# Performance work log

Hardware: AMD Instinct MI355X
Metric: run time of the kernel (lower is better)

## Reference

```python
import jax, jax.numpy as jnp
import numpy as np

WIDTH = 1024
NH = 16
HD = 64
MBS = 16
B = 4
L = 2048
BASE_LR = 1.0
EPS = 1e-6


def gelu_tanh(x):
    return jax.nn.gelu(x, approximate=True)


def gelu_bwd(x):
    t = jnp.tanh(0.79788456 * x * (1 + 0.044715 * x * x))
    return 0.5 * x * ((1 - t * t) * (0.79788456 + 0.1070322243 * x * x)) + 0.5 * (1 + t)


def ln_fwd(x, g, b):
    mu = x.mean(-1, keepdims=True)
    var = ((x - mu) ** 2).mean(-1, keepdims=True)
    return g * ((x - mu) * jax.lax.rsqrt(var + EPS)) + b


def ln_l2_bwd(x, tgt, g, b):
    # grad of 0.5*||LN(x)-tgt||^2 wrt x
    mu = x.mean(-1, keepdims=True)
    var = ((x - mu) ** 2).mean(-1, keepdims=True)
    std = jnp.sqrt(var + EPS)
    xh = (x - mu) / std
    gx = (g * xh + b - tgt) * g
    return (gx - gx.mean(-1, keepdims=True) - xh * (gx * xh).mean(-1, keepdims=True)) / std


def adapter_forward(hidden_states, Wq, Wk, Wv, Wo, Wg, lr_w, lr_b,
                    learnable_token_idx, norm_w, norm_b, W1, b1, W2, b2,
                    post_w, post_b):
    Bb, Ll, width = hidden_states.shape
    nh, hd = norm_w.shape
    mbs = learnable_token_idx.shape[0]
    nc = Ll // mbs  # L chosen divisible by mini_batch_size

    def split_heads(x):  # [B,L,width] -> [B,nh,nc,mbs,hd]
        return x.reshape(Bb, Ll, nh, hd).transpose(0, 2, 1, 3).reshape(Bb, nh, nc, mbs, hd)

    XQ = split_heads(hidden_states @ Wq.T)
    XK = split_heads(hidden_states @ Wk.T)
    XV = split_heads(hidden_states @ Wv.T)

    # eta: learnable per-token lr gate (get_eta)
    X = hidden_states.reshape(Bb, nc, mbs, width)
    lr = jnp.einsum('bnkc,hdc->bhnkd', X, lr_w) + lr_b.reshape(1, nh, 1, 1, 1)
    lr = jax.nn.sigmoid(lr).transpose(0, 1, 2, 4, 3)  # [B,nh,nc,1,mbs]
    lr_eta = BASE_LR * lr / hd
    token_idx = jnp.clip(1.0 / jnp.arange(1, mbs + 1, dtype=hidden_states.dtype)
                         + learnable_token_idx, 0.0, None)
    token_eta = token_idx.reshape(1, 1, 1, mbs, 1)
    eta = token_eta * lr_eta  # [B,nh,nc,mbs,mbs]

    tril = jnp.tril(jnp.ones((mbs, mbs), dtype=hidden_states.dtype))
    lnw = norm_w.reshape(nh, 1, hd)
    lnb = norm_b.reshape(nh, 1, hd)

    def step(carry, xs):
        W1s, b1s, W2s, b2s = carry  # [B,nh,hd,4hd], [B,nh,1,4hd], [B,nh,4hd,hd], [B,nh,1,hd]
        XQm, XKm, XVm, etam = xs    # [B,nh,mbs,hd] x3, [B,nh,mbs,mbs]
        X1 = XKm
        Z1 = X1 @ W1s + b1s
        X2 = gelu_tanh(Z1)
        Z2 = X2 @ W2s + b2s
        gZ2 = ln_l2_bwd(Z2, XVm - XKm, lnw, lnb)
        gZ1 = (gZ2 @ jnp.swapaxes(W2s, -1, -2)) * gelu_bwd(Z1)
        eta_tril = etam * tril
        Attn1 = tril * (XQm @ jnp.swapaxes(X1, -1, -2))
        b1_bar = b1s - eta_tril @ gZ1
        Z1_bar = XQm @ W1s - (etam * Attn1) @ gZ1 + b1_bar
        X2_bar = gelu_tanh(Z1_bar)
        Attn2 = tril * (X2_bar @ jnp.swapaxes(X2, -1, -2))
        b2_bar = b2s - eta_tril @ gZ2
        Z2_bar = X2_bar @ W2s - (etam * Attn2) @ gZ2 + b2_bar
        last = etam[:, :, -1, :, None]  # [B,nh,mbs,1]
        W1n = W1s - jnp.swapaxes(last * X1, -1, -2) @ gZ1
        b1n = b1s - (last * gZ1).sum(-2, keepdims=True)
        W2n = W2s - jnp.swapaxes(last * X2, -1, -2) @ gZ2
        b2n = b2s - (last * gZ2).sum(-2, keepdims=True)
        XQW = XQm + ln_fwd(Z2_bar, lnw, lnb)
        return (W1n, b1n, W2n, b2n), XQW

    carry0 = (jnp.broadcast_to(W1, (Bb,) + W1.shape),
              jnp.broadcast_to(b1, (Bb,) + b1.shape),
              jnp.broadcast_to(W2, (Bb,) + W2.shape),
              jnp.broadcast_to(b2, (Bb,) + b2.shape))
    xs = tuple(jnp.moveaxis(t, 2, 0) for t in (XQ, XK, XV, eta))
    _, XQW = jax.lax.scan(step, carry0, xs)  # [nc,B,nh,mbs,hd]
    out = XQW.transpose(1, 0, 3, 2, 4).reshape(Bb, Ll, width)

    # post_norm (LayerNorm eps=1e-6)
    out = ln_fwd(out, post_w, post_b)
    # gate
    out = gelu_tanh(hidden_states @ Wg.T) * out
    # o_proj
    return out @ Wo.T


def setup_inputs():
    key = jax.random.key(0)
    ks = jax.random.split(key, 10)
    n = lambda k, s: jax.random.normal(k, s, dtype=jnp.float32) * 0.02
    return {
        'hidden_states': jax.random.normal(ks[0], (B, L, WIDTH), dtype=jnp.float32),
        'Wq': n(ks[1], (WIDTH, WIDTH)),
        'Wk': n(ks[2], (WIDTH, WIDTH)),
        'Wv': n(ks[3], (WIDTH, WIDTH)),
        'Wo': n(ks[4], (WIDTH, WIDTH)),
        'Wg': n(ks[5], (WIDTH, WIDTH)),
        'lr_w': n(ks[6], (NH, 1, WIDTH)),
        'lr_b': jnp.zeros((NH, 1), jnp.float32),
        'learnable_token_idx': jnp.zeros((MBS,), jnp.float32),
        'norm_w': jnp.ones((NH, HD), jnp.float32),
        'norm_b': jnp.zeros((NH, HD), jnp.float32),
        'W1': n(ks[7], (NH, HD, 4 * HD)),
        'b1': jnp.zeros((NH, 1, 4 * HD), jnp.float32),
        'W2': n(ks[8], (NH, 4 * HD, HD)),
        'b2': jnp.zeros((NH, 1, HD), jnp.float32),
        'post_w': jnp.ones((WIDTH,), jnp.float32),
        'post_b': jnp.zeros((WIDTH,), jnp.float32),
    }


def reference(hidden_states, Wq, Wk, Wv, Wo, Wg, lr_w, lr_b, learnable_token_idx,
              norm_w, norm_b, W1, b1, W2, b2, post_w, post_b):
    return adapter_forward(hidden_states, Wq, Wk, Wv, Wo, Wg, lr_w, lr_b,
                           learnable_token_idx, norm_w, norm_b, W1, b1, W2, b2,
                           post_w, post_b)
```

## Files before the change

kernel.cpp:

```cpp
#include <hip/hip_runtime.h>

#define WIDTH 1024
#define MBSZ 16
#define LLL 2048
#define NCHUNK 128

typedef __attribute__((ext_vector_type(4))) float f32x4;
typedef __attribute__((ext_vector_type(2))) float f32x2;
typedef __attribute__((ext_vector_type(8))) short short8;
typedef __attribute__((ext_vector_type(4))) short short4v;
typedef __attribute__((ext_vector_type(2))) unsigned u32x2;
typedef __attribute__((ext_vector_type(4))) unsigned u32x4;

#define MFMA16(a, b, c) __builtin_amdgcn_mfma_f32_16x16x32_bf16((a), (b), (c), 0, 0, 0)

__device__ __forceinline__ short f2bf(float f) {
  unsigned u = __float_as_uint(f);
  u = (u + 0x7FFFu + ((u >> 16) & 1u)) >> 16;
  return (short)u;
}
__device__ __forceinline__ float bf2f(short s) {
  return __uint_as_float(((unsigned)(unsigned short)s) << 16);
}
__device__ __forceinline__ unsigned cvt_pk(float lo, float hi) {
  unsigned r;
  asm("v_cvt_pk_bf16_f32 %0, %1, %2" : "=v"(r) : "v"(lo), "v"(hi));
  return r;
}
__device__ __forceinline__ float fast_e2u(float x) {
  return __builtin_amdgcn_exp2f(x * (2.30220776f + 0.10294322f * x * x));
}
__device__ __forceinline__ float gelu_f(float x) {
  float e = fast_e2u(x);
  return x * (1.0f - __builtin_amdgcn_rcpf(e + 1.0f));
}
__device__ __forceinline__ float gelu_bwd_f(float x) {
  float e = fast_e2u(x);
  float r = __builtin_amdgcn_rcpf(e + 1.0f);
  return 2.0f * x * r * (1.0f - r) * (0.79788456f + 0.1070322243f * x * x) + (1.0f - r);
}
__device__ __forceinline__ int w2row(int d) { return d * 264 + (d >> 3) * 24; }

template <int OUTBF>
__device__ __forceinline__ void gemm_64x128(const short* __restrict__ A,
                                            const short* __restrict__ W,
                                            float* __restrict__ C,
                                            short* __restrict__ Cb,
                                            int m0, int n0,
                                            short* sA, short* sB, int t2) {
  const int wv = t2 >> 6, ln = t2 & 63;
  const int fr = ln & 15, kh = (ln >> 4) * 8;
  const int arow = t2 >> 2, aseg = (t2 & 3) * 8;
  f32x4 acc[8];
#pragma unroll
  for (int s = 0; s < 8; ++s) acc[s] = (f32x4){0.f, 0.f, 0.f, 0.f};
  const short* ga = A + (long)(m0 + arow) * 1024 + aseg;
  const short* gw0 = W + (long)(n0 + arow) * 1024 + aseg;
  const short* gw1 = W + (long)(n0 + 64 + arow) * 1024 + aseg;
  for (int k0 = 0; k0 < 1024; k0 += 32) {
    const short8 a8 = *(const short8*)(ga + k0);
    const short8 w80 = *(const short8*)(gw0 + k0);
    const short8 w81 = *(const short8*)(gw1 + k0);
    *(short8*)&sA[arow * 40 + aseg] = a8;
    *(short8*)&sB[arow * 40 + aseg] = w80;
    *(short8*)&sB[(arow + 64) * 40 + aseg] = w81;
    __syncthreads();
    const short8 af = *(const short8*)&sA[(wv * 16 + fr) * 40 + kh];
#pragma unroll
    for (int s = 0; s < 8; ++s) {
      const short8 bf8 = *(const short8*)&sB[(s * 16 + fr) * 40 + kh];
      acc[s] = MFMA16(af, bf8, acc[s]);
    }
    __syncthreads();
  }
  const int orow = m0 + wv * 16 + (ln >> 4) * 4;
#pragma unroll
  for (int s = 0; s < 8; ++s)
#pragma unroll
    for (int q = 0; q < 4; ++q) {
      const long off = (long)(orow + q) * 1024 + n0 + s * 16 + fr;
      if (OUTBF) Cb[off] = f2bf(acc[s][q]);
      else C[off] = acc[s][q];
    }
}

__global__ __launch_bounds__(256) void cvt_kernel(const float* __restrict__ hs,
                                                  const float* __restrict__ Wq,
                                                  const float* __restrict__ Wk,
                                                  const float* __restrict__ Wv,
                                                  const float* __restrict__ Wg,
                                                  const float* __restrict__ Wo,
                                                  short* __restrict__ dst) {
  const long idx = ((long)blockIdx.x * 256 + threadIdx.x) * 8;
  if (idx >= 13631488L) return;
  const float* src;
  long off;
  if (idx < 8388608L)       { src = hs; off = idx; }
  else if (idx < 9437184L)  { src = Wq; off = idx - 8388608L; }
  else if (idx < 10485760L) { src = Wk; off = idx - 9437184L; }
  else if (idx < 11534336L) { src = Wv; off = idx - 10485760L; }
  else if (idx < 12582912L) { src = Wg; off = idx - 11534336L; }
  else                      { src = Wo; off = idx - 12582912L; }
  const f32x4 a = *(const f32x4*)(src + off);
  const f32x4 b = *(const f32x4*)(src + off + 4);
  u32x4 o;
  o[0] = cvt_pk(a[0], a[1]); o[1] = cvt_pk(a[2], a[3]);
  o[2] = cvt_pk(b[0], b[1]); o[3] = cvt_pk(b[2], b[3]);
  *(u32x4*)(dst + idx) = o;
}

__global__ __launch_bounds__(256) void gemm_final(const short* __restrict__ A,
                                                  const short* __restrict__ W,
                                                  float* __restrict__ C) {
  __shared__ __align__(16) short sA[2560];
  __shared__ __align__(16) short sB[5120];
  gemm_64x128<0>(A, W, C, nullptr, blockIdx.x * 64, blockIdx.y * 128, sA, sB, threadIdx.x);
}

__global__ __launch_bounds__(256) void qkv_lr_kernel(const short* __restrict__ hsb,
                                                     const short* __restrict__ Wqb,
                                                     const short* __restrict__ Wkb,
                                                     const short* __restrict__ Wvb,
                                                     float* __restrict__ Qb,
                                                     float* __restrict__ Kb,
                                                     float* __restrict__ Vb,
                                                     const float* __restrict__ hs,
                                                     const float* __restrict__ lrw,
                                                     const float* __restrict__ lrb,
                                                     float* __restrict__ LRb) {
  __shared__ __align__(16) short sA[2560];
  __shared__ __align__(16) short sB[5120];
  __shared__ __align__(16) float row[1024];
  const int tid = threadIdx.x;
  const int idx = blockIdx.x;
  if (idx < 3072) {
    const int which = idx >> 10, t = idx & 1023;
    const short* W = (which == 0) ? Wqb : (which == 1) ? Wkb : Wvb;
    float* C = (which == 0) ? Qb : (which == 1) ? Kb : Vb;
    gemm_64x128<0>(hsb, W, C, nullptr, (t & 127) * 64, (t >> 7) * 128, sA, sB, tid);
  } else {
    const int t = idx - 3072;
    *(f32x4*)&row[tid * 4] = *(const f32x4*)&hs[(long)t * 1024 + tid * 4];
    __syncthreads();
    const int hh = tid >> 4, j = tid & 15;
    const float* wrow = lrw + hh * 1024;
    float s = 0.f;
#pragma unroll 4
    for (int m = 0; m < 16; ++m) {
      const int c = j * 4 + m * 64;
      f32x4 x = *(const f32x4*)&row[c];
      f32x4 w = *(const f32x4*)&wrow[c];
      s += x[0] * w[0] + x[1] * w[1] + x[2] * w[2] + x[3] * w[3];
    }
#pragma unroll
    for (int o = 8; o; o >>= 1) s += __shfl_xor(s, o, 16);
    if (j == 0) {
      const float v = s + lrb[hh];
      const float sg = 1.f / (1.f + expf(-v));
      const int b = t >> 11, tr = t & 2047;
      LRb[((b << 4) + hh) * 2048 + tr] = sg * (1.f / 64.f);
    }
  }
}

__global__ __launch_bounds__(512, 2) void scan_gate_kernel(
    float* __restrict__ Qb, const float* __restrict__ Kb, const float* __restrict__ Vb,
    const float* __restrict__ LRb, const float* __restrict__ lti,
    const float* __restrict__ nw, const float* __restrict__ nb,
    const float* __restrict__ W1in, const float* __restrict__ b1in,
    const float* __restrict__ W2in, const float* __restrict__ b2in,
    const short* __restrict__ hsA, const short* __restrict__ Wgb,
    short* __restrict__ Gout) {
  __shared__ __align__(16) short sW1b[256 * 72];
  __shared__ __align__(16) short sW2dp[64 * 264 + 192];
  __shared__ __align__(16) short la1T[64 * 24];
  __shared__ __align__(16) short la2T[256 * 24];
  __shared__ __align__(16) short sX1b[16 * 72];
  __shared__ __align__(16) short sXQb[16 * 72];
  __shared__ __align__(16) float sXQf[16 * 68];
  __shared__ __align__(16) float sTg[16 * 72];
  __shared__ __align__(16) short sX2b[16 * 264];
  __shared__ __align__(16) short sXbb[16 * 264];
  __shared__ __align__(16) short sG1c[256 * 24];
  __shared__ __align__(16) short sG2b[16 * 72];
  __shared__ __align__(16) short sG2c[64 * 24];
  __shared__ __align__(16) float sZ2p0[16 * 68];
  __shared__ __align__(16) float sZ2p1[16 * 68];
  __shared__ __align__(16) float sZ2f[16 * 68];
  __shared__ __align__(16) short sC1b[16 * 24];
  __shared__ __align__(16) short sC2b[16 * 24];
  __shared__ __align__(16) float sB1[256];
  __shared__ __align__(16) float sB2[64];
  __shared__ float sLr[16];
  __shared__ float sTok[16];
  __shared__ __align__(16) float sLnw[64];
  __shared__ __align__(16) float sLnb[64];

  const int tid = threadIdx.x;

  if (blockIdx.x >= 64) {
    const int hh = tid >> 8, t2 = tid & 255;
    const int tile = (blockIdx.x - 64) * 2 + hh;
    short* sAh = sW1b + hh * 7680;
    short* sBh = sAh + 2560;
    gemm_64x128<1>(hsA, Wgb, nullptr, Gout, (tile & 127) * 64, (tile >> 7) * 128, sAh, sBh, t2);
    return;
  }

  const int bh = blockIdx.x, b = bh >> 4, h = bh & 15;
  const int w = tid >> 6, ln = tid & 63;
  const int fr = ln & 15, half = ln >> 4, hk = half * 8;
  const int nt0 = 2 * w;

  float w1m[8][4], w2m[8][4];
#pragma unroll
  for (int r = 0; r < 8; ++r) {
    const int T = w * 8 + r, dt = T >> 4, pt = T & 15;
#pragma unroll
    for (int qq = 0; qq < 4; ++qq) {
      w1m[r][qq] = W1in[h * 16384 + (dt * 16 + half * 4 + qq) * 256 + pt * 16 + fr];
      w2m[r][qq] = W2in[h * 16384 + (pt * 16 + half * 4 + qq) * 64 + dt * 16 + fr];
    }
  }
  for (int e = tid; e < 16384; e += 512) {
    {
      const int d = e >> 8, p = e & 255;
      sW1b[p * 72 + d] = f2bf(W1in[h * 16384 + e]);
    }
    {
      const int p = e >> 6, d = e & 63;
      sW2dp[w2row(d) + (p ^ (((d >> 3) & 3) << 3))] = f2bf(W2in[h * 16384 + e]);
    }
  }
  if (tid < 256) sB1[tid] = b1in[h * 256 + tid];
  if (tid < 64) { sB2[tid] = b2in[h * 64 + tid]; sLnw[tid] = nw[h * 64 + tid]; sLnb[tid] = nb[h * 64 + tid]; }
  if (tid < 16) sTok[tid] = fmaxf(1.0f / (float)(tid + 1) + lti[tid], 0.0f);

  const f32x4 zf4 = (f32x4){0.f, 0.f, 0.f, 0.f};
  short8 zs8;
#pragma unroll
  for (int j = 0; j < 8; ++j) zs8[j] = 0;

  const int pf_i = tid >> 5;
  const int pf_d = (tid & 31) * 2;
  f32x2 pk, pq, pv;
  float plr = 0.f;
  {
    const long a0 = ((long)(b * LLL + pf_i)) * WIDTH + h * 64 + pf_d;
    pk = *(const f32x2*)&Kb[a0];
    pq = *(const f32x2*)&Qb[a0];
    pv = *(const f32x2*)&Vb[a0];
    if (tid < 16) plr = LRb[(long)bh * 2048 + tid];
  }

  for (int n = 0; n < NCHUNK; ++n) {
    const long gbase = ((long)(b * LLL + n * MBSZ)) * WIDTH + h * 64;

    {
      *(unsigned*)&sX1b[pf_i * 72 + pf_d] = cvt_pk(pk[0], pk[1]);
      *(unsigned*)&sXQb[pf_i * 72 + pf_d] = cvt_pk(pq[0], pq[1]);
      sXQf[pf_i * 68 + pf_d] = pq[0];
      sXQf[pf_i * 68 + pf_d + 1] = pq[1];
      sTg[pf_i * 72 + pf_d] = pv[0] - pk[0];
      sTg[pf_i * 72 + pf_d + 1] = pv[1] - pk[1];
      if (tid < 16) sLr[tid] = plr;
    }
    __syncthreads();

    short8 aX1[2], aXQ[2];
    aX1[0] = *(const short8*)&sX1b[fr * 72 + hk];
    aX1[1] = *(const short8*)&sX1b[fr * 72 + 32 + hk];
    aXQ[0] = *(const short8*)&sXQb[fr * 72 + hk];
    aXQ[1] = *(const short8*)&sXQb[fr * 72 + 32 + hk];
    f32x4 z1[2], q1[2];
    float b1p[2];
#pragma unroll
    for (int t = 0; t < 2; ++t) {
      const int p = (nt0 + t) * 16 + fr;
      z1[t] = zf4; q1[t] = zf4;
#pragma unroll
      for (int ks = 0; ks < 2; ++ks) {
        short8 bw = *(const short8*)&sW1b[p * 72 + ks * 32 + hk];
        z1[t] = MFMA16(aX1[ks], bw, z1[t]);
        q1[t] = MFMA16(aXQ[ks], bw, q1[t]);
      }
      b1p[t] = sB1[p];
#pragma unroll
      for (int qq = 0; qq < 4; ++qq) {
        z1[t][qq] += b1p[t];
        sX2b[(half * 4 + qq) * 264 + p] = f2bf(gelu_f(z1[t][qq]));
      }
    }
    {
      const float tok15 = sTok[15];
      const int d = tid >> 3, j0 = (tid & 7) * 2;
      const float v0 = bf2f(sX1b[j0 * 72 + d]) * (tok15 * sLr[j0]);
      const float v1 = bf2f(sX1b[(j0 + 1) * 72 + d]) * (tok15 * sLr[j0 + 1]);
      *(unsigned*)&la1T[d * 24 + j0] = cvt_pk(v0, v1);
    }
    if (w == 0) {
      f32x4 c = MFMA16(aXQ[0], aX1[0], zf4);
      c = MFMA16(aXQ[1], aX1[1], c);
#pragma unroll
      for (int qq = 0; qq < 4; ++qq) {
        const int i = half * 4 + qq, j = fr;
        sC1b[i * 24 + j] = f2bf((i >= j) ? sTok[i] * sLr[j] * (c[qq] + 1.0f) : 0.0f);
      }
    }
    __syncthreads();

    float bb2old = 0.f;
    {
      const int dt = w & 3, k2 = w >> 2;
      const int d = dt * 16 + fr;
      const int sw = ((d >> 3) & 3) << 3;
      const int rb = w2row(d);
      f32x4 za = zf4, zb = zf4;
#pragma unroll
      for (int ks = k2 * 4; ks < k2 * 4 + 2; ++ks) {
        short8 a = *(const short8*)&sX2b[fr * 264 + ks * 32 + hk];
        short8 bfr = *(const short8*)&sW2dp[rb + ((ks * 32 + hk) ^ sw)];
        za = MFMA16(a, bfr, za);
      }
#pragma unroll
      for (int ks = k2 * 4 + 2; ks < k2 * 4 + 4; ++ks) {
        short8 a = *(const short8*)&sX2b[fr * 264 + ks * 32 + hk];
        short8 bfr = *(const short8*)&sW2dp[rb + ((ks * 32 + hk) ^ sw)];
        zb = MFMA16(a, bfr, zb);
      }
      float* dst = k2 ? sZ2p1 : sZ2p0;
#pragma unroll
      for (int qq = 0; qq < 4; ++qq)
        dst[(half * 4 + qq) * 68 + d] = za[qq] + zb[qq];
      if (w < 4) bb2old = sB2[w * 16 + fr];
    }
    __syncthreads();

    {
      const int i = tid >> 5, j2 = tid & 31;
      const int e0 = j2 * 2;
      const f32x2 zp0 = *(const f32x2*)&sZ2p0[i * 68 + e0];
      const f32x2 zp1 = *(const f32x2*)&sZ2p1[i * 68 + e0];
      const f32x2 b2v = *(const f32x2*)&sB2[e0];
      f32x2 z;
      z[0] = zp0[0] + zp1[0] + b2v[0];
      z[1] = zp0[1] + zp1[1] + b2v[1];
      float s1 = z[0] + z[1];
      float s2 = z[0] * z[0] + z[1] * z[1];
#pragma unroll
      for (int o = 16; o; o >>= 1) { s1 += __shfl_xor(s1, o, 32); s2 += __shfl_xor(s2, o, 32); }
      const float mu = s1 * (1.f / 64.f);
      const float rstd = rsqrtf(s2 * (1.f / 64.f) - mu * mu + 1e-6f);
      const f32x2 g = *(const f32x2*)&sLnw[e0];
      const f32x2 bb = *(const f32x2*)&sLnb[e0];
      const f32x2 tg = *(const f32x2*)&sTg[i * 72 + e0];
      f32x2 xh, gx;
      float a1 = 0.f, a2 = 0.f;
#pragma unroll
      for (int e = 0; e < 2; ++e) {
        xh[e] = (z[e] - mu) * rstd;
        gx[e] = (g[e] * xh[e] + bb[e] - tg[e]) * g[e];
        a1 += gx[e]; a2 += gx[e] * xh[e];
      }
#pragma unroll
      for (int o = 16; o; o >>= 1) { a1 += __shfl_xor(a1, o, 32); a2 += __shfl_xor(a2, o, 32); }
      const float m1 = a1 * (1.f / 64.f), m2 = a2 * (1.f / 64.f);
      const float o0 = (gx[0] - m1 - xh[0] * m2) * rstd;
      const float o1 = (gx[1] - m1 - xh[1] * m2) * rstd;
      const unsigned lo = cvt_pk(o0, o1);
      *(unsigned*)&sG2b[i * 72 + e0] = lo;
      sG2c[(e0 + 0) * 24 + i] = (short)lo;
      sG2c[(e0 + 1) * 24 + i] = (short)(lo >> 16);
    }
    __syncthreads();

    {
      short8 aG2[2];
      aG2[0] = *(const short8*)&sG2b[fr * 72 + hk];
      aG2[1] = *(const short8*)&sG2b[fr * 72 + 32 + hk];
#pragma unroll
      for (int t = 0; t < 2; ++t) {
        const int p = (nt0 + t) * 16 + fr;
        f32x4 g = zf4;
#pragma unroll
        for (int ks = 0; ks < 2; ++ks) {
          const int dg = ks * 32 + hk;
          const int rb2 = w2row(dg) + (p ^ (((dg >> 3) & 3) << 3));
          short8 bw;
#pragma unroll
          for (int jj = 0; jj < 8; ++jj) bw[jj] = sW2dp[rb2 + jj * 264];
          g = MFMA16(aG2[ks], bw, g);
        }
        const unsigned lo = cvt_pk(g[0] * gelu_bwd_f(z1[t][0]), g[1] * gelu_bwd_f(z1[t][1]));
        const unsigned hi = cvt_pk(g[2] * gelu_bwd_f(z1[t][2]), g[3] * gelu_bwd_f(z1[t][3]));
        *(u32x2*)&sG1c[p * 24 + half * 4] = (u32x2){lo, hi};
      }
    }
    if (tid < 64) {
      float s = 0.f;
#pragma unroll
      for (int k = 0; k < 4; ++k) {
        const short4v g4 = *(const short4v*)&sG2c[tid * 24 + k * 4];
        const f32x4 lr4 = *(const f32x4*)&sLr[k * 4];
        s += lr4[0] * bf2f(g4[0]) + lr4[1] * bf2f(g4[1]) +
             lr4[2] * bf2f(g4[2]) + lr4[3] * bf2f(g4[3]);
      }
      sB2[tid] -= sTok[15] * s;
    }
    __syncthreads();

    {
      short8 ac = zs8;
      if (half < 2) ac = *(const short8*)&sC1b[fr * 24 + hk];
#pragma unroll
      for (int t = 0; t < 2; ++t) {
        const int p = (nt0 + t) * 16 + fr;
        short8 bg = zs8;
        if (half < 2) bg = *(const short8*)&sG1c[p * 24 + hk];
        f32x4 corr = MFMA16(ac, bg, zf4);
#pragma unroll
        for (int qq = 0; qq < 4; ++qq)
          sXbb[(half * 4 + qq) * 264 + p] = f2bf(gelu_f(q1[t][qq] + b1p[t] - corr[qq]));
      }
    }
    {
#pragma unroll
      for (int r = 0; r < 8; ++r) {
        const int T = w * 8 + r, dt = T >> 4, pt = T & 15;
        short8 af = zs8, bg = zs8;
        if (half < 2) {
          af = *(const short8*)&la1T[(dt * 16 + fr) * 24 + hk];
          bg = *(const short8*)&sG1c[(pt * 16 + fr) * 24 + hk];
        }
        f32x4 dl = MFMA16(af, bg, zf4);
        const int pp = pt * 16 + fr, d0 = dt * 16 + half * 4;
        w1m[r][0] -= dl[0]; w1m[r][1] -= dl[1]; w1m[r][2] -= dl[2]; w1m[r][3] -= dl[3];
        const unsigned lo = cvt_pk(w1m[r][0], w1m[r][1]);
        const unsigned hi = cvt_pk(w1m[r][2], w1m[r][3]);
        *(u32x2*)&sW1b[pp * 72 + d0] = (u32x2){lo, hi};
      }
    }
    if (tid < 256) {
      float s = 0.f;
#pragma unroll
      for (int k = 0; k < 4; ++k) {
        const short4v g4 = *(const short4v*)&sG1c[tid * 24 + k * 4];
        const f32x4 lr4 = *(const f32x4*)&sLr[k * 4];
        s += lr4[0] * bf2f(g4[0]) + lr4[1] * bf2f(g4[1]) +
             lr4[2] * bf2f(g4[2]) + lr4[3] * bf2f(g4[3]);
      }
      sB1[tid] -= sTok[15] * s;
    }
    __syncthreads();

    {
      const int nn = (n + 1 < NCHUNK) ? n + 1 : n;
      const long a1 = ((long)(b * LLL + nn * MBSZ + pf_i)) * WIDTH + h * 64 + pf_d;
      pk = *(const f32x2*)&Kb[a1];
      pq = *(const f32x2*)&Qb[a1];
      pv = *(const f32x2*)&Vb[a1];
      if (tid < 16) plr = LRb[(long)bh * 2048 + nn * MBSZ + tid];
    }
    f32x4 zbar = zf4;
    if (w < 4) {
      const int d = w * 16 + fr;
      const int sw = ((d >> 3) & 3) << 3;
      const int rb = w2row(d);
      f32x4 za = zf4, zb = zf4;
#pragma unroll
      for (int ks = 0; ks < 4; ++ks) {
        short8 a = *(const short8*)&sXbb[fr * 264 + ks * 32 + hk];
        short8 bfr = *(const short8*)&sW2dp[rb + ((ks * 32 + hk) ^ sw)];
        za = MFMA16(a, bfr, za);
      }
#pragma unroll
      for (int ks = 4; ks < 8; ++ks) {
        short8 a = *(const short8*)&sXbb[fr * 264 + ks * 32 + hk];
        short8 bfr = *(const short8*)&sW2dp[rb + ((ks * 32 + hk) ^ sw)];
        zb = MFMA16(a, bfr, zb);
      }
      zbar[0] = za[0] + zb[0]; zbar[1] = za[1] + zb[1];
      zbar[2] = za[2] + zb[2]; zbar[3] = za[3] + zb[3];
    } else if (w == 4) {
      f32x4 c = zf4;
#pragma unroll
      for (int ks = 0; ks < 8; ++ks) {
        short8 a = *(const short8*)&sXbb[fr * 264 + ks * 32 + hk];
        short8 bx = *(const short8*)&sX2b[fr * 264 + ks * 32 + hk];
        c = MFMA16(a, bx, c);
      }
#pragma unroll
      for (int qq = 0; qq < 4; ++qq) {
        const int i = half * 4 + qq, j = fr;
        sC2b[i * 24 + j] = f2bf((i >= j) ? sTok[i] * sLr[j] * (c[qq] + 1.0f) : 0.0f);
      }
    } else {
      const float tok15 = sTok[15];
      for (int pp = tid - 320; pp < 256; pp += 192) {
        unsigned uu[8];
#pragma unroll
        for (int jp = 0; jp < 8; ++jp) {
          const float v0 = bf2f(sX2b[(2 * jp) * 264 + pp]) * (tok15 * sLr[2 * jp]);
          const float v1 = bf2f(sX2b[(2 * jp + 1) * 264 + pp]) * (tok15 * sLr[2 * jp + 1]);
          uu[jp] = cvt_pk(v0, v1);
        }
        *(u32x4*)&la2T[pp * 24] = (u32x4){uu[0], uu[1], uu[2], uu[3]};
        *(u32x4*)&la2T[pp * 24 + 8] = (u32x4){uu[4], uu[5], uu[6], uu[7]};
      }
    }
    __syncthreads();

    if (w < 4) {
      const int d = w * 16 + fr;
      short8 ac = zs8, bg = zs8;
      if (half < 2) {
        ac = *(const short8*)&sC2b[fr * 24 + hk];
        bg = *(const short8*)&sG2c[d * 24 + hk];
      }
      f32x4 corr = MFMA16(ac, bg, zf4);
#pragma unroll
      for (int qq = 0; qq < 4; ++qq)
        sZ2f[(half * 4 + qq) * 68 + d] = zbar[qq] + bb2old - corr[qq];
    }
    {
#pragma unroll
      for (int r = 0; r < 8; ++r) {
        const int T = w * 8 + r, pt = T & 15, dt = T >> 4;
        short8 af = zs8, bg = zs8;
        if (half < 2) {
          af = *(const short8*)&la2T[(pt * 16 + fr) * 24 + hk];
          bg = *(const short8*)&sG2c[(dt * 16 + fr) * 24 + hk];
        }
        f32x4 dl = MFMA16(af, bg, zf4);
        const int dd = dt * 16 + fr;
        const int swp = ((dd >> 3) & 3) << 3;
        const int p0 = pt * 16 + half * 4;
        w2m[r][0] -= dl[0]; w2m[r][1] -= dl[1]; w2m[r][2] -= dl[2]; w2m[r][3] -= dl[3];
        const unsigned lo = cvt_pk(w2m[r][0], w2m[r][1]);
        const unsigned hi = cvt_pk(w2m[r][2], w2m[r][3]);
        *(u32x2*)&sW2dp[w2row(dd) + (p0 ^ swp)] = (u32x2){lo, hi};
      }
    }
    __syncthreads();

    {
      const int i = tid >> 5, j2 = tid & 31;
      const int e0 = j2 * 2;
      const f32x2 z = *(const f32x2*)&sZ2f[i * 68 + e0];
      float s1 = z[0] + z[1];
      float s2 = z[0] * z[0] + z[1] * z[1];
#pragma unroll
      for (int o = 16; o; o >>= 1) { s1 += __shfl_xor(s1, o, 32); s2 += __shfl_xor(s2, o, 32); }
      const float mu = s1 * (1.f / 64.f);
      const float rstd = rsqrtf(s2 * (1.f / 64.f) - mu * mu + 1e-6f);
      const f32x2 g = *(const f32x2*)&sLnw[e0];
      const f32x2 bb = *(const f32x2*)&sLnb[e0];
      const f32x2 xq = *(const f32x2*)&sXQf[i * 68 + e0];
      f32x2 o2;
      o2[0] = xq[0] + g[0] * ((z[0] - mu) * rstd) + bb[0];
      o2[1] = xq[1] + g[1] * ((z[1] - mu) * rstd) + bb[1];
      *(f32x2*)&Qb[gbase + (long)i * WIDTH + e0] = o2;
    }
    __syncthreads();
  }
}

__global__ __launch_bounds__(256) void epi_kernel(const float* __restrict__ X,
                                                  const short* __restrict__ G,
                                                  const float* __restrict__ pw,
                                                  const float* __restrict__ pb,
                                                  short* __restrict__ T) {
  __shared__ float red[8];
  const int t = blockIdx.x, tid = threadIdx.x;
  const long base = (long)t * 1024 + tid * 4;
  f32x4 x = *(const f32x4*)&X[base];
  float s1 = x[0] + x[1] + x[2] + x[3];
  float s2 = x[0] * x[0] + x[1] * x[1] + x[2] * x[2] + x[3] * x[3];
#pragma unroll
  for (int o = 32; o; o >>= 1) { s1 += __shfl_xor(s1, o, 64); s2 += __shfl_xor(s2, o, 64); }
  const int wv = tid >> 6, ln = tid & 63;
  if (ln == 0) { red[wv] = s1; red[4 + wv] = s2; }
  __syncthreads();
  s1 = red[0] + red[1] + red[2] + red[3];
  s2 = red[4] + red[5] + red[6] + red[7];
  const float mu = s1 * (1.f / 1024.f);
  const float rstd = rsqrtf(s2 * (1.f / 1024.f) - mu * mu + 1e-6f);
  const short4v g4 = *(const short4v*)&G[base];
  f32x4 w = *(const f32x4*)&pw[tid * 4];
  f32x4 bb = *(const f32x4*)&pb[tid * 4];
  float o4[4];
#pragma unroll
  for (int e = 0; e < 4; ++e) {
    float y = w[e] * ((x[e] - mu) * rstd) + bb[e];
    o4[e] = gelu_f(bf2f(g4[e])) * y;
  }
  *(u32x2*)&T[base] = (u32x2){cvt_pk(o4[0], o4[1]), cvt_pk(o4[2], o4[3])};
}

extern "C" void kernel_launch(void* const* d_in, const int* in_sizes, int n_in,
                              void* d_out, int out_size, void* d_ws, size_t ws_size,
                              hipStream_t stream) {
  const float* hs  = (const float*)d_in[0];
  const float* Wq  = (const float*)d_in[1];
  const float* Wk  = (const float*)d_in[2];
  const float* Wv  = (const float*)d_in[3];
  const float* Wo  = (const float*)d_in[4];
  const float* Wg  = (const float*)d_in[5];
  const float* lrw = (const float*)d_in[6];
  const float* lrb = (const float*)d_in[7];
  const float* lti = (const float*)d_in[8];
  const float* nw  = (const float*)d_in[9];
  const float* nb  = (const float*)d_in[10];
  const float* W1  = (const float*)d_in[11];
  const float* b1  = (const float*)d_in[12];
  const float* W2  = (const float*)d_in[13];
  const float* b2  = (const float*)d_in[14];
  const float* pw  = (const float*)d_in[15];
  const float* pb  = (const float*)d_in[16];
  float* out = (float*)d_out;
  float* ws = (float*)d_ws;

  float* Qb  = ws;
  float* Kb  = ws + 8388608;
  float* Vb  = ws + 16777216;
  float* LRb = ws + 25165824;
  short* hsb = (short*)(ws + 25296896);
  short* Wqb = hsb + 8388608;
  short* Wkb = Wqb + 1048576;
  short* Wvb = Wkb + 1048576;
  short* Wgb = Wvb + 1048576;
  short* Wob = Wgb + 1048576;
  short* Tb  = (short*)Kb;
  short* Gbb = (short*)out;

  cvt_kernel<<<6656, 256, 0, stream>>>(hs, Wq, Wk, Wv, Wg, Wo, hsb);
  qkv_lr_kernel<<<11264, 256, 0, stream>>>(hsb, Wqb, Wkb, Wvb, Qb, Kb, Vb, hs, lrw, lrb, LRb);
  scan_gate_kernel<<<576, 512, 0, stream>>>(Qb, Kb, Vb, LRb, lti, nw, nb, W1, b1, W2, b2,
                                            hsb, Wgb, Gbb);
  epi_kernel<<<8192, 256, 0, stream>>>(Qb, Gbb, pw, pb, Tb);
  gemm_final<<<dim3(128, 8), 256, 0, stream>>>(Tb, Wob, out);
}
```

Measured before the change: 953.4 us.

## Rebalance per-chunk W2 forward, LN backward, and la2T prep across warps

The W2 forward GEMM now runs on 4 warps, each covering the full K range, instead of 8 warps with a split-K partial sum. This drops the two partial buffers and adds the bias directly into sZ2f. The two layer-norm phases now use 256 threads with 4-wide vector loads and stores, and 16-lane shuffles. The freed threads 256+ build the la2T transposed operand in that same phase, which removes it from a later stage. The aim is fewer shared-memory round trips and better overlap inside the serial scan, at the cost of idle warps during the W2 GEMM.

```diff
diff --git a/kernel.cpp b/kernel.cpp
--- a/kernel.cpp
+++ b/kernel.cpp
@@ -184,8 +184,6 @@
   __shared__ __align__(16) short sG1c[256 * 24];
   __shared__ __align__(16) short sG2b[16 * 72];
   __shared__ __align__(16) short sG2c[64 * 24];
-  __shared__ __align__(16) float sZ2p0[16 * 68];
-  __shared__ __align__(16) float sZ2p1[16 * 68];
   __shared__ __align__(16) float sZ2f[16 * 68];
   __shared__ __align__(16) short sC1b[16 * 24];
   __shared__ __align__(16) short sC2b[16 * 24];
@@ -310,67 +308,75 @@
     __syncthreads();
 
     float bb2old = 0.f;
-    {
-      const int dt = w & 3, k2 = w >> 2;
-      const int d = dt * 16 + fr;
+    if (w < 4) {
+      const int d = w * 16 + fr;
       const int sw = ((d >> 3) & 3) << 3;
       const int rb = w2row(d);
       f32x4 za = zf4, zb = zf4;
 #pragma unroll
-      for (int ks = k2 * 4; ks < k2 * 4 + 2; ++ks) {
+      for (int ks = 0; ks < 4; ++ks) {
         short8 a = *(const short8*)&sX2b[fr * 264 + ks * 32 + hk];
         short8 bfr = *(const short8*)&sW2dp[rb + ((ks * 32 + hk) ^ sw)];
         za = MFMA16(a, bfr, za);
       }
 #pragma unroll
-      for (int ks = k2 * 4 + 2; ks < k2 * 4 + 4; ++ks) {
+      for (int ks = 4; ks < 8; ++ks) {
         short8 a = *(const short8*)&sX2b[fr * 264 + ks * 32 + hk];
         short8 bfr = *(const short8*)&sW2dp[rb + ((ks * 32 + hk) ^ sw)];
         zb = MFMA16(a, bfr, zb);
       }
-      float* dst = k2 ? sZ2p1 : sZ2p0;
+      bb2old = sB2[d];
 #pragma unroll
       for (int qq = 0; qq < 4; ++qq)
-        dst[(half * 4 + qq) * 68 + d] = za[qq] + zb[qq];
-      if (w < 4) bb2old = sB2[w * 16 + fr];
-    }
-    __syncthreads();
-
-    {
-      const int i = tid >> 5, j2 = tid & 31;
-      const int e0 = j2 * 2;
-      const f32x2 zp0 = *(const f32x2*)&sZ2p0[i * 68 + e0];
-      const f32x2 zp1 = *(const f32x2*)&sZ2p1[i * 68 + e0];
-      const f32x2 b2v = *(const f32x2*)&sB2[e0];
-      f32x2 z;
-      z[0] = zp0[0] + zp1[0] + b2v[0];
-      z[1] = zp0[1] + zp1[1] + b2v[1];
-      float s1 = z[0] + z[1];
-      float s2 = z[0] * z[0] + z[1] * z[1];
-#pragma unroll
-      for (int o = 16; o; o >>= 1) { s1 += __shfl_xor(s1, o, 32); s2 += __shfl_xor(s2, o, 32); }
+        sZ2f[(half * 4 + qq) * 68 + d] = za[qq] + zb[qq] + bb2old;
+    }
+    __syncthreads();
+
+    if (tid < 256) {
+      const int i = tid >> 4, j4 = tid & 15;
+      const f32x4 z = *(const f32x4*)&sZ2f[i * 68 + j4 * 4];
+      float s1 = z[0] + z[1] + z[2] + z[3];
+      float s2 = z[0] * z[0] + z[1] * z[1] + z[2] * z[2] + z[3] * z[3];
+#pragma unroll
+      for (int o = 8; o; o >>= 1) { s1 += __shfl_xor(s1, o, 16); s2 += __shfl_xor(s2, o, 16); }
       const float mu = s1 * (1.f / 64.f);
       const float rstd = rsqrtf(s2 * (1.f / 64.f) - mu * mu + 1e-6f);
-      const f32x2 g = *(const f32x2*)&sLnw[e0];
-      const f32x2 bb = *(const f32x2*)&sLnb[e0];
-      const f32x2 tg = *(const f32x2*)&sTg[i * 72 + e0];
-      f32x2 xh, gx;
+      const f32x4 g = *(const f32x4*)&sLnw[j4 * 4];
+      const f32x4 bb = *(const f32x4*)&sLnb[j4 * 4];
+      const f32x4 tg = *(const f32x4*)&sTg[i * 72 + j4 * 4];
+      f32x4 xh, gx;
       float a1 = 0.f, a2 = 0.f;
 #pragma unroll
-      for (int e = 0; e < 2; ++e) {
+      for (int e = 0; e < 4; ++e) {
         xh[e] = (z[e] - mu) * rstd;
         gx[e] = (g[e] * xh[e] + bb[e] - tg[e]) * g[e];
         a1 += gx[e]; a2 += gx[e] * xh[e];
       }
 #pragma unroll
-      for (int o = 16; o; o >>= 1) { a1 += __shfl_xor(a1, o, 32); a2 += __shfl_xor(a2, o, 32); }
+      for (int o = 8; o; o >>= 1) { a1 += __shfl_xor(a1, o, 16); a2 += __shfl_xor(a2, o, 16); }
       const float m1 = a1 * (1.f / 64.f), m2 = a2 * (1.f / 64.f);
-      const float o0 = (gx[0] - m1 - xh[0] * m2) * rstd;
-      const float o1 = (gx[1] - m1 - xh[1] * m2) * rstd;
-      const unsigned lo = cvt_pk(o0, o1);
-      *(unsigned*)&sG2b[i * 72 + e0] = lo;
-      sG2c[(e0 + 0) * 24 + i] = (short)lo;
-      sG2c[(e0 + 1) * 24 + i] = (short)(lo >> 16);
+      float o4[4];
+#pragma unroll
+      for (int e = 0; e < 4; ++e) o4[e] = (gx[e] - m1 - xh[e] * m2) * rstd;
+      const unsigned lo = cvt_pk(o4[0], o4[1]);
+      const unsigned hi = cvt_pk(o4[2], o4[3]);
+      *(u32x2*)&sG2b[i * 72 + j4 * 4] = (u32x2){lo, hi};
+      sG2c[(j4 * 4 + 0) * 24 + i] = (short)lo;
+      sG2c[(j4 * 4 + 1) * 24 + i] = (short)(lo >> 16);
+      sG2c[(j4 * 4 + 2) * 24 + i] = (short)hi;
+      sG2c[(j4 * 4 + 3) * 24 + i] = (short)(hi >> 16);
+    } else {
+      const int pp = tid - 256;
+      const float tok15 = sTok[15];
+      unsigned uu[8];
+#pragma unroll
+      for (int jp = 0; jp < 8; ++jp) {
+        const float v0 = bf2f(sX2b[(2 * jp) * 264 + pp]) * (tok15 * sLr[2 * jp]);
+        const float v1 = bf2f(sX2b[(2 * jp + 1) * 264 + pp]) * (tok15 * sLr[2 * jp + 1]);
+        uu[jp] = cvt_pk(v0, v1);
+      }
+      *(u32x4*)&la2T[pp * 24] = (u32x4){uu[0], uu[1], uu[2], uu[3]};
+      *(u32x4*)&la2T[pp * 24 + 8] = (u32x4){uu[4], uu[5], uu[6], uu[7]};
     }
     __syncthreads();
 
@@ -493,19 +499,6 @@
       for (int qq = 0; qq < 4; ++qq) {
         const int i = half * 4 + qq, j = fr;
         sC2b[i * 24 + j] = f2bf((i >= j) ? sTok[i] * sLr[j] * (c[qq] + 1.0f) : 0.0f);
-      }
-    } else {
-      const float tok15 = sTok[15];
-      for (int pp = tid - 320; pp < 256; pp += 192) {
-        unsigned uu[8];
-#pragma unroll
-        for (int jp = 0; jp < 8; ++jp) {
-          const float v0 = bf2f(sX2b[(2 * jp) * 264 + pp]) * (tok15 * sLr[2 * jp]);
-          const float v1 = bf2f(sX2b[(2 * jp + 1) * 264 + pp]) * (tok15 * sLr[2 * jp + 1]);
-          uu[jp] = cvt_pk(v0, v1);
-        }
-        *(u32x4*)&la2T[pp * 24] = (u32x4){uu[0], uu[1], uu[2], uu[3]};
-        *(u32x4*)&la2T[pp * 24 + 8] = (u32x4){uu[4], uu[5], uu[6], uu[7]};
       }
     }
     __syncthreads();
@@ -543,23 +536,22 @@
     }
     __syncthreads();
 
-    {
-      const int i = tid >> 5, j2 = tid & 31;
-      const int e0 = j2 * 2;
-      const f32x2 z = *(const f32x2*)&sZ2f[i * 68 + e0];
-      float s1 = z[0] + z[1];
-      float s2 = z[0] * z[0] + z[1] * z[1];
-#pragma unroll
-      for (int o = 16; o; o >>= 1) { s1 += __shfl_xor(s1, o, 32); s2 += __shfl_xor(s2, o, 32); }
+    if (tid < 256) {
+      const int i = tid >> 4, j4 = tid & 15;
+      const f32x4 z = *(const f32x4*)&sZ2f[i * 68 + j4 * 4];
+      float s1 = z[0] + z[1] + z[2] + z[3];
+      float s2 = z[0] * z[0] + z[1] * z[1] + z[2] * z[2] + z[3] * z[3];
+#pragma unroll
+      for (int o = 8; o; o >>= 1) { s1 += __shfl_xor(s1, o, 16); s2 += __shfl_xor(s2, o, 16); }
       const float mu = s1 * (1.f / 64.f);
       const float rstd = rsqrtf(s2 * (1.f / 64.f) - mu * mu + 1e-6f);
-      const f32x2 g = *(const f32x2*)&sLnw[e0];
-      const f32x2 bb = *(const f32x2*)&sLnb[e0];
-      const f32x2 xq = *(const f32x2*)&sXQf[i * 68 + e0];
-      f32x2 o2;
-      o2[0] = xq[0] + g[0] * ((z[0] - mu) * rstd) + bb[0];
-      o2[1] = xq[1] + g[1] * ((z[1] - mu) * rstd) + bb[1];
-      *(f32x2*)&Qb[gbase + (long)i * WIDTH + e0] = o2;
+      const f32x4 g = *(const f32x4*)&sLnw[j4 * 4];
+      const f32x4 bb = *(const f32x4*)&sLnb[j4 * 4];
+      const f32x4 xq = *(const f32x4*)&sXQf[i * 68 + j4 * 4];
+      f32x4 o4;
+#pragma unroll
+      for (int e = 0; e < 4; ++e) o4[e] = xq[e] + g[e] * ((z[e] - mu) * rstd) + bb[e];
+      *(f32x4*)&Qb[gbase + (long)i * WIDTH + j4 * 4] = o4;
     }
     __syncthreads();
   }
```

New measurement: 918.1 us, median of 2. 1.04x faster.
